# Optimization experiments

Measured on AMD Instinct MI355X. Metric: run time of the kernel, lower is better.

The kernel has to match this reference:

```python
import jax, jax.numpy as jnp
import numpy as np


def setup_inputs() -> dict:
    key = jax.random.key(0)
    k1, k2 = jax.random.split(key)
    B, S, H = 16, 512, 512
    x = jax.random.normal(k1, (B, S, H), dtype=jnp.float32)
    durations = jax.random.randint(k2, (B, S), 0, 16, dtype=jnp.int32)
    return {"x": x, "durations": durations, "max_len": 4096}


def reference(x, durations, max_len):
    # x: [B, S, H] float, durations: [B, S] int, max_len: python int
    B, S, H = x.shape
    # Inclusive cumulative end positions of each token's expanded span.
    cum = jnp.cumsum(durations, axis=1)                      # [B, S]
    t = jnp.arange(max_len, dtype=cum.dtype)                 # [T]
    # For output frame t, source token j is the first with cum[j] > t.
    idx = jax.vmap(lambda c: jnp.searchsorted(c, t, side='right'))(cum)  # [B, T]
    valid = idx < S                                          # frames beyond total stay zero
    idx_c = jnp.minimum(idx, S - 1)
    out = jnp.take_along_axis(x, idx_c[:, :, None], axis=1)  # [B, T, H]
    return jnp.where(valid[:, :, None], out, jnp.zeros((), dtype=x.dtype))
```

## Files before the change

### kernel.cpp

```cpp
#include <hip/hip_runtime.h>
#include <hip/hip_bf16.h>

#define SCAN_BLOCK 512

typedef __attribute__((ext_vector_type(4))) float f32x4;

__global__ __launch_bounds__(SCAN_BLOCK)
void lr_buildmap_kernel(const int* __restrict__ dur, int* __restrict__ map,
                        const int* __restrict__ T_ptr, int BS, int BT) {
    const int T = *T_ptr;
    const int B = BT / T;
    const int S = BS / B;
    __shared__ int sdata[SCAN_BLOCK];
    const int tid = threadIdx.x;
    for (int row = blockIdx.x; row < B; row += gridDim.x) {
        int carry = 0;
        for (int base = 0; base < S; base += SCAN_BLOCK) {
            const int n = min(SCAN_BLOCK, S - base);
            __syncthreads();
            const int v = (tid < n) ? dur[row * S + base + tid] : 0;
            sdata[tid] = v;
            __syncthreads();
            #pragma unroll
            for (int off = 1; off < SCAN_BLOCK; off <<= 1) {
                int add = (tid >= off) ? sdata[tid - off] : 0;
                __syncthreads();
                sdata[tid] += add;
                __syncthreads();
            }
            if (tid < n) {
                const int inc   = sdata[tid] + carry;
                const int end   = min(inc, T);
                const int start = min(inc - v, T);
                const int tok   = row * S + base + tid;
                for (int t = start; t < end; ++t) map[row * T + t] = tok;
            }
            carry += sdata[SCAN_BLOCK - 1];
        }
        __syncthreads();
        const int total = min(carry, T);
        for (int t = total + tid; t < T; t += SCAN_BLOCK) map[row * T + t] = -1;
    }
}

__global__ __launch_bounds__(256)
void lr_expand_kernel(const f32x4* __restrict__ x, const int* __restrict__ map,
                      f32x4* __restrict__ out, int n4, int shift) {
    const int g = blockIdx.x * blockDim.x + threadIdx.x;
    if (g >= n4) return;
    const int frame = g >> shift;
    const int lane  = g & ((1 << shift) - 1);
    const int tok   = map[frame];
    f32x4 v = (f32x4)(0.f, 0.f, 0.f, 0.f);
    if (tok >= 0) v = x[((size_t)tok << shift) + lane];
    __builtin_nontemporal_store(v, &out[g]);
}

extern "C" void kernel_launch(void* const* d_in, const int* in_sizes, int n_in,
                              void* d_out, int out_size, void* d_ws, size_t ws_size,
                              hipStream_t stream) {
    const float* x     = (const float*)d_in[0];
    const int*   dur   = (const int*)d_in[1];
    const int*   T_ptr = (const int*)d_in[2];

    const int BSH = in_sizes[0];
    const int BS  = in_sizes[1];
    const int H   = BSH / BS;
    const int BT  = out_size / H;
    const int H4  = H / 4;
    const int shift = __builtin_ctz(H4);

    int* map = (int*)d_ws;

    lr_buildmap_kernel<<<64, SCAN_BLOCK, 0, stream>>>(dur, map, T_ptr, BS, BT);

    const int n4 = out_size / 4;
    const int grid = (n4 + 255) / 256;
    lr_expand_kernel<<<grid, 256, 0, stream>>>((const f32x4*)x, map, (f32x4*)d_out,
                                               n4, shift);
}
```

Baseline: 170.4 us.

## Use wavefront shuffle scan and per-frame binary search to build map

Replaces the shared-memory Hillis-Steele block scan with a wave-level shuffle scan plus a small cross-wave offset pass, keeping the full cumulative array in LDS. The map is then built by having each thread binary-search that array for its output frames, instead of each token thread writing its own span serially. This is meant to remove the many block barriers and the load imbalance of variable-length per-token writes, and to make map writes coalesced. It limits S to 4096 because of the fixed LDS array, and adds log(S) LDS reads per frame.

After: 173.5 us. Within noise of the previous version (+1.8%).

```diff
diff --git a/kernel.cpp b/kernel.cpp
--- a/kernel.cpp
+++ b/kernel.cpp
@@ -1,45 +1,56 @@
 #include <hip/hip_runtime.h>
 #include <hip/hip_bf16.h>
 
-#define SCAN_BLOCK 512
-
 typedef __attribute__((ext_vector_type(4))) float f32x4;
 
-__global__ __launch_bounds__(SCAN_BLOCK)
+#define MAXS 4096
+
+__global__ __launch_bounds__(512)
 void lr_buildmap_kernel(const int* __restrict__ dur, int* __restrict__ map,
                         const int* __restrict__ T_ptr, int BS, int BT) {
     const int T = *T_ptr;
     const int B = BT / T;
     const int S = BS / B;
-    __shared__ int sdata[SCAN_BLOCK];
-    const int tid = threadIdx.x;
+    __shared__ int scum[MAXS];
+    __shared__ int wtot[9];
+    const int tid  = threadIdx.x;
+    const int lane = tid & 63;
+    const int wv   = tid >> 6;
+    const int nw   = blockDim.x >> 6;
+
     for (int row = blockIdx.x; row < B; row += gridDim.x) {
         int carry = 0;
-        for (int base = 0; base < S; base += SCAN_BLOCK) {
-            const int n = min(SCAN_BLOCK, S - base);
+        for (int base = 0; base < S; base += blockDim.x) {
+            const int j = base + tid;
             __syncthreads();
-            const int v = (tid < n) ? dur[row * S + base + tid] : 0;
-            sdata[tid] = v;
+            int v = (j < S) ? dur[row * S + j] : 0;
+            int sum = v;
+            #pragma unroll
+            for (int off = 1; off < 64; off <<= 1) {
+                int n = __shfl_up(sum, off, 64);
+                if (lane >= off) sum += n;
+            }
+            if (lane == 63) wtot[wv] = sum;
             __syncthreads();
-            #pragma unroll
-            for (int off = 1; off < SCAN_BLOCK; off <<= 1) {
-                int add = (tid >= off) ? sdata[tid - off] : 0;
-                __syncthreads();
-                sdata[tid] += add;
-                __syncthreads();
+            if (tid == 0) {
+                int acc = 0;
+                for (int w = 0; w < nw; ++w) { int t0 = wtot[w]; wtot[w] = acc; acc += t0; }
             }
-            if (tid < n) {
-                const int inc   = sdata[tid] + carry;
-                const int end   = min(inc, T);
-                const int start = min(inc - v, T);
-                const int tok   = row * S + base + tid;
-                for (int t = start; t < end; ++t) map[row * T + t] = tok;
-            }
-            carry += sdata[SCAN_BLOCK - 1];
+            __syncthreads();
+            const int chunk_off = wtot[wv];
+            if (j < S) scum[j] = sum + chunk_off + carry;
+            __syncthreads();
+            carry = scum[min(base + (int)blockDim.x, S) - 1];
         }
         __syncthreads();
-        const int total = min(carry, T);
-        for (int t = total + tid; t < T; t += SCAN_BLOCK) map[row * T + t] = -1;
+        for (int t = tid; t < T; t += blockDim.x) {
+            int lo = 0, hi = S;
+            while (lo < hi) {
+                int mid = (lo + hi) >> 1;
+                if (scum[mid] <= t) lo = mid + 1; else hi = mid;
+            }
+            map[row * T + t] = (lo < S) ? (row * S + lo) : -1;
+        }
     }
 }
 
@@ -72,7 +83,7 @@
 
     int* map = (int*)d_ws;
 
-    lr_buildmap_kernel<<<64, SCAN_BLOCK, 0, stream>>>(dur, map, T_ptr, BS, BT);
+    lr_buildmap_kernel<<<64, 512, 0, stream>>>(dur, map, T_ptr, BS, BT);
 
     const int n4 = out_size / 4;
     const int grid = (n4 + 255) / 256;
```
